# Kernel tuning notes

Hardware: AMD Instinct MI355X
Metric: run time of the kernel (lower is better)

Reference implementation:

```python
import jax, jax.numpy as jnp
import numpy as np

N, D, P, NS = 2048, 64, 32, 512  # nnodes, stop_embedding_size, preference_dim, n_active_stops
LEAKY_SLOPE = 0.01
COS_EPS = 1e-8


def setup_inputs() -> dict:
    key = jax.random.key(0)
    ks = jax.random.split(key, 10)
    dist = jax.random.uniform(ks[0], (N, N), dtype=jnp.float32)
    stops = jax.random.randint(ks[1], (NS,), 0, N)
    emb_w = jax.random.normal(ks[2], (N, D), dtype=jnp.float32) * 0.05      # nn.Embedding weight
    lin_l_w = jax.random.normal(ks[3], (P, D), dtype=jnp.float32) * 0.05    # SAGEConv lin_l (aggregated)
    lin_l_b = jnp.zeros((P,), dtype=jnp.float32)
    lin_r_w = jax.random.normal(ks[4], (P, D), dtype=jnp.float32) * 0.05    # SAGEConv lin_r (root)
    edge_w = jax.random.normal(ks[5], (2 * P,), dtype=jnp.float32) * 0.05   # edge_summarizer weight
    edge_b = jnp.zeros((), dtype=jnp.float32)
    in_len = 2 * N + 3 + P
    comb_w = jax.random.normal(ks[6], (N, in_len), dtype=jnp.float32) * 0.02  # combiner weight
    comb_b = jnp.zeros((N,), dtype=jnp.float32)
    return {
        "dist": dist, "emb_w": emb_w,
        "lin_l_w": lin_l_w, "lin_l_b": lin_l_b, "lin_r_w": lin_r_w,
        "edge_w": edge_w, "edge_b": edge_b,
        "comb_w": comb_w, "comb_b": comb_b,
        "stops": stops, "weekday": 3, "vehicles": 5,
    }


def reference(dist, emb_w, lin_l_w, lin_l_b, lin_r_w, edge_w, edge_b,
              comb_w, comb_b, stops, weekday, vehicles):
    dt = emb_w.dtype
    # --- cosine-similarity graph build ---
    norm = jnp.maximum(jnp.linalg.norm(emb_w, axis=1, keepdims=True), COS_EPS)
    xn = emb_w / norm
    sim = xn @ xn.T                                   # [N, N]
    sim = sim * (1.0 - jnp.eye(N, dtype=dt))          # fill_diagonal_(0)
    keep = jnp.zeros((N,), dtype=bool).at[stops].set(True)
    adj = ((sim > 0.5) & keep[:, None] & keep[None, :]).astype(dt)  # [N, N]
    # --- SAGEConv (mean aggregation): lin_l(mean_j x_j) + lin_r(x_i) ---
    deg = jnp.maximum(adj.sum(axis=1, keepdims=True), 1.0)
    agg = (adj @ emb_w) / deg                         # [N, D]
    pref = agg @ lin_l_w.T + lin_l_b + emb_w @ lin_r_w.T   # [N, P]
    # --- all-pairs edge summaries: Linear([pref_i, pref_j]) + LeakyReLU ---
    # equivalent to concat-then-linear, without materializing [N^2, 2P]
    a = pref @ edge_w[:P]                             # [N]
    b = pref @ edge_w[P:]                             # [N]
    es = a[:, None] + b[None, :] + edge_b             # [N, N]
    es = jnp.where(es >= 0, es, LEAKY_SLOPE * es)
    # --- combiner + log-softmax ---
    weekday_feat = jnp.full((N, 1), weekday, dtype=dt)
    vehicle_feat = jnp.full((N, 1), vehicles, dtype=dt)
    stop_feat = keep.astype(dt)[:, None]
    combined = jnp.concatenate([pref, es, dist, weekday_feat, vehicle_feat, stop_feat], axis=1)
    out = combined @ comb_w.T + comb_b                # [N, N]
    return jax.nn.log_softmax(out, axis=1)
```

## Files before the change

### kernel.cpp

```cpp
#include <hip/hip_runtime.h>

typedef unsigned short u16;
typedef __attribute__((ext_vector_type(8))) short bf16x8;
typedef __attribute__((ext_vector_type(4))) float f32x4;

__device__ __forceinline__ u16 f2bf(float f) {
    return (u16)((__float_as_uint(f) + 0x8000u) >> 16);
}

#define N_NODES 2048
#define D_EMB 64
#define P_DIM 32
#define NS_STOPS 512
#define IN_LEN 4131
#define NKT 65
#define NKTA 33

#define SWZ(row, c) ((((row) * 8) + ((c) ^ ((row) & 7))) * 8)

__device__ __forceinline__ void gload16(const u16* g, u16* l) {
    __builtin_amdgcn_global_load_lds((const __attribute__((address_space(1))) void*)g,
                                     (__attribute__((address_space(3))) void*)l, 16, 0, 0);
}

__global__ __launch_bounds__(256) void k_aggpref(const float* __restrict__ emb, const int* __restrict__ stops,
                                                 const float* __restrict__ lin_l_w, const float* __restrict__ lin_l_b,
                                                 const float* __restrict__ lin_r_w, const float* __restrict__ edge_w,
                                                 float* __restrict__ pref, float* __restrict__ av, float* __restrict__ bv) {
    __shared__ float se[NS_STOPS][68];
    __shared__ int bm[64];
    __shared__ int kl[NS_STOPS];
    __shared__ float nrm[NS_STOPS];
    __shared__ float xiS[8][D_EMB];
    __shared__ float aggS[8][D_EMB];
    __shared__ float niS[8];
    __shared__ int degS[8];
    __shared__ int kiS[8];
    __shared__ int cnt;
    int t = threadIdx.x;
    int i0 = blockIdx.x * 8;
    if (t < 64) bm[t] = 0;
    if (t == 0) cnt = 0;
    if (t < 8) degS[t] = 0;
    ((float*)aggS)[t] = 0.f;
    ((float*)aggS)[t + 256] = 0.f;
    __syncthreads();
    {
        int s0 = stops[t], s1 = stops[t + 256];
        atomicOr(&bm[s0 >> 5], 1 << (s0 & 31));
        atomicOr(&bm[s1 >> 5], 1 << (s1 & 31));
    }
    __syncthreads();
    {
        int w = bm[t >> 2];
        int base = (t >> 2) * 32 + (t & 3) * 8;
        #pragma unroll
        for (int e = 0; e < 8; ++e)
            if ((w >> ((t & 3) * 8 + e)) & 1) { int p = atomicAdd(&cnt, 1); kl[p] = base + e; }
    }
    if (t < 8) { int i = i0 + t; kiS[t] = (bm[i >> 5] >> (i & 31)) & 1; }
    {
        int n = t >> 5, d = (t & 31) * 2;
        xiS[n][d]     = emb[(i0 + n) * D_EMB + d];
        xiS[n][d + 1] = emb[(i0 + n) * D_EMB + d + 1];
    }
    __syncthreads();
    int nk = cnt;
    for (int u = t >> 3; u < nk; u += 32) {
        int l8 = (t & 7) * 8;
        f32x4 a = *(const f32x4*)&emb[kl[u] * D_EMB + l8];
        f32x4 b = *(const f32x4*)&emb[kl[u] * D_EMB + l8 + 4];
        *(f32x4*)&se[u][l8] = a;
        *(f32x4*)&se[u][l8 + 4] = b;
    }
    if (t < 8) {
        float s = 0.f;
        #pragma unroll
        for (int d = 0; d < D_EMB; ++d) s += xiS[t][d] * xiS[t][d];
        niS[t] = fmaxf(sqrtf(s), 1e-8f);
    }
    __syncthreads();
    for (int u = t; u < nk; u += 256) {
        float s = 0.f;
        #pragma unroll
        for (int d = 0; d < 16; ++d) {
            f32x4 v = *(const f32x4*)&se[u][d * 4];
            s += v[0] * v[0] + v[1] * v[1] + v[2] * v[2] + v[3] * v[3];
        }
        nrm[u] = fmaxf(sqrtf(s), 1e-8f);
    }
    __syncthreads();
    for (int u = t; u < nk; u += 256) {
        int j = kl[u];
        float nj = nrm[u];
        f32x4 er[16];
        #pragma unroll
        for (int d = 0; d < 16; ++d) er[d] = *(const f32x4*)&se[u][d * 4];
        #pragma unroll
        for (int n = 0; n < 8; ++n) {
            if (!kiS[n] || j == i0 + n) continue;
            f32x4 dv = {0.f, 0.f, 0.f, 0.f};
            #pragma unroll
            for (int d = 0; d < 16; ++d) dv += (*(const f32x4*)&xiS[n][d * 4]) * er[d];
            float dot = dv[0] + dv[1] + dv[2] + dv[3];
            if (dot > 0.5f * niS[n] * nj) {
                atomicAdd(&degS[n], 1);
                #pragma unroll
                for (int d = 0; d < 16; ++d) {
                    atomicAdd(&aggS[n][d * 4 + 0], er[d][0]);
                    atomicAdd(&aggS[n][d * 4 + 1], er[d][1]);
                    atomicAdd(&aggS[n][d * 4 + 2], er[d][2]);
                    atomicAdd(&aggS[n][d * 4 + 3], er[d][3]);
                }
            }
        }
    }
    __syncthreads();
    {
        int n = t >> 5, p = t & 31;
        int i = i0 + n;
        float inv = kiS[n] ? (1.f / fmaxf((float)degS[n], 1.0f)) : 0.f;
        float s = lin_l_b[p];
        const float* wl = &lin_l_w[p * D_EMB];
        const float* wr = &lin_r_w[p * D_EMB];
        #pragma unroll
        for (int d = 0; d < D_EMB; ++d) s += aggS[n][d] * inv * wl[d] + xiS[n][d] * wr[d];
        pref[i * P_DIM + p] = s;
        float a = s * edge_w[p];
        float b = s * edge_w[P_DIM + p];
        #pragma unroll
        for (int off = 16; off; off >>= 1) { a += __shfl_xor(a, off, 32); b += __shfl_xor(b, off, 32); }
        if (p == 0) { av[i] = a; bv[i] = b; }
    }
}

__global__ __launch_bounds__(256) void k_pack(const float* __restrict__ comb_w, const float* __restrict__ comb_b,
                                              const int* __restrict__ wk_p, const int* __restrict__ vh_p,
                                              const float* __restrict__ dist, const float* __restrict__ pref,
                                              u16* __restrict__ Bp, u16* __restrict__ Ap,
                                              float* __restrict__ cvec, float* __restrict__ w3) {
    int kt = blockIdx.x;
    int ty = blockIdx.y;
    int t = threadIdx.x;
    if (ty < 16) {
        int nt = ty;
        u16* tb = Bp + ((size_t)nt * NKT + kt) * 8192;
        #pragma unroll
        for (int it = 0; it < 4; ++it) {
            int q = t + it * 256;
            int r = q >> 3, c = q & 7;
            int j = nt * 128 + r;
            int k0 = kt * 64 + c * 8;
            const float* cw = comb_w + (size_t)j * IN_LEN;
            bf16x8 v;
            if (k0 < 4096) {
                f32x4 f0, f1;
                __builtin_memcpy(&f0, cw + 32 + k0, 16);
                __builtin_memcpy(&f1, cw + 36 + k0, 16);
                #pragma unroll
                for (int e = 0; e < 4; ++e) { v[e] = (short)f2bf(f0[e]); v[4 + e] = (short)f2bf(f1[e]); }
            } else if (k0 < 4128) {
                f32x4 f0, f1;
                __builtin_memcpy(&f0, cw + (k0 - 4096), 16);
                __builtin_memcpy(&f1, cw + (k0 - 4092), 16);
                #pragma unroll
                for (int e = 0; e < 4; ++e) { v[e] = (short)f2bf(f0[e]); v[4 + e] = (short)f2bf(f1[e]); }
            } else {
                #pragma unroll
                for (int e = 0; e < 8; ++e) v[e] = 0;
            }
            *(bf16x8*)&tb[r * 64 + ((c ^ (r & 7)) * 8)] = v;
        }
        if (kt == 64 && t < 128) {
            int j = nt * 128 + t;
            const float* cw = comb_w + (size_t)j * IN_LEN;
            float wk = (float)wk_p[0], vh = (float)vh_p[0];
            cvec[j] = wk * cw[4128] + vh * cw[4129] + comb_b[j];
            w3[j] = cw[4130];
        }
    } else {
        if (kt < 32) return;
        int rt = ty - 16;
        u16* ta = Ap + ((size_t)rt * NKTA + (kt - 32)) * 4096;
        #pragma unroll
        for (int it = 0; it < 2; ++it) {
            int q = t + it * 256;
            int r = q >> 3, c = q & 7;
            int row = rt * 64 + r;
            int k0 = kt * 64 + c * 8;
            bf16x8 v;
            if (k0 < 4096) {
                const f32x4* dp = (const f32x4*)(dist + (size_t)row * 2048 + (k0 - 2048));
                f32x4 f0 = dp[0], f1 = dp[1];
                #pragma unroll
                for (int e = 0; e < 4; ++e) { v[e] = (short)f2bf(f0[e]); v[4 + e] = (short)f2bf(f1[e]); }
            } else if (k0 < 4128) {
                const f32x4* pp = (const f32x4*)(pref + (size_t)row * P_DIM + (k0 - 4096));
                f32x4 f0 = pp[0], f1 = pp[1];
                #pragma unroll
                for (int e = 0; e < 4; ++e) { v[e] = (short)f2bf(f0[e]); v[4 + e] = (short)f2bf(f1[e]); }
            } else {
                #pragma unroll
                for (int e = 0; e < 8; ++e) v[e] = 0;
            }
            *(bf16x8*)&ta[r * 64 + ((c ^ (r & 7)) * 8)] = v;
        }
    }
}

__global__ __launch_bounds__(256, 4) void k_gemm_d(const u16* __restrict__ Ap, const u16* __restrict__ Bp,
                                                   const float* __restrict__ av, const float* __restrict__ bv,
                                                   const float* __restrict__ edge_b,
                                                   float* __restrict__ Cout) {
    __shared__ __attribute__((aligned(16))) short As[2][4096];
    __shared__ __attribute__((aligned(16))) short Bs[2][4096];
    int t = threadIdx.x;
    int b = blockIdx.x;
    int c = b & 7, u = b >> 3;
    int mt = (c & 1) * 16 + (u & 15);
    int nt = (c >> 1) * 8 + (u >> 4);
    int tileM = mt * 64, tileN = nt * 64;
    int lane = t & 63;
    int wid = t >> 6;
    int waveM = wid & 1, waveN = wid >> 1;
    int l16 = lane & 15, quad = lane >> 4;
    int r_ = t >> 2;
    float avr = av[tileM + r_] + edge_b[0];

    f32x4 acc[2][2];
    #pragma unroll
    for (int a_ = 0; a_ < 2; ++a_)
        #pragma unroll
        for (int b_ = 0; b_ < 2; ++b_) acc[a_][b_] = (f32x4){0.f, 0.f, 0.f, 0.f};

    const u16* gB = Bp + ((size_t)(nt >> 1) * NKT) * 8192 + (nt & 1) * 4096 + t * 8;
    const u16* gA = Ap + ((size_t)mt * NKTA) * 4096 + t * 8;

#define ISSUE(ktv, bb) do { \
        const u16* b0 = gB + (size_t)(ktv) * 8192; \
        u16* bd = (u16*)Bs[bb] + t * 8; \
        gload16(b0, bd); \
        gload16(b0 + 2048, bd + 2048); \
        if ((ktv) < 32) { \
            int k0 = (ktv) * 64; \
            _Pragma("unroll") \
            for (int cc = 0; cc < 2; ++cc) { \
                int ch = (t & 3) * 2 + cc; \
                f32x4 f0 = *(const f32x4*)&bv[k0 + ch * 8]; \
                f32x4 f1 = *(const f32x4*)&bv[k0 + ch * 8 + 4]; \
                bf16x8 v; \
                _Pragma("unroll") \
                for (int e = 0; e < 4; ++e) { \
                    float s0 = avr + f0[e]; s0 = (s0 >= 0.f) ? s0 : 0.01f * s0; \
                    float s1 = avr + f1[e]; s1 = (s1 >= 0.f) ? s1 : 0.01f * s1; \
                    v[e] = (short)f2bf(s0); v[4 + e] = (short)f2bf(s1); \
                } \
                *(bf16x8*)&As[bb][SWZ(r_, ch)] = v; \
            } \
        } else { \
            const u16* a0 = gA + (size_t)((ktv) - 32) * 4096; \
            u16* ad = (u16*)As[bb] + t * 8; \
            gload16(a0, ad); \
            gload16(a0 + 2048, ad + 2048); \
        } \
    } while (0)

    ISSUE(0, 0);

    int cur = 0;
    for (int kt = 0; kt < NKT; ++kt) {
        __syncthreads();
        if (kt + 1 < NKT) ISSUE(kt + 1, cur ^ 1);
        const short* Asc = As[cur];
        const short* Bsc = Bs[cur];
        #pragma unroll
        for (int kk = 0; kk < 64; kk += 32) {
            int cbase = kk >> 3;
            bf16x8 af[2], bfr[2];
            #pragma unroll
            for (int mi = 0; mi < 2; ++mi) {
                int row = waveM * 32 + mi * 16 + l16;
                af[mi] = *(const bf16x8*)&Asc[SWZ(row, cbase + quad)];
            }
            #pragma unroll
            for (int ni = 0; ni < 2; ++ni) {
                int row = waveN * 32 + ni * 16 + l16;
                bfr[ni] = *(const bf16x8*)&Bsc[SWZ(row, cbase + quad)];
            }
            #pragma unroll
            for (int mi = 0; mi < 2; ++mi)
                #pragma unroll
                for (int ni = 0; ni < 2; ++ni)
                    acc[mi][ni] = __builtin_amdgcn_mfma_f32_16x16x32_bf16(af[mi], bfr[ni], acc[mi][ni], 0, 0, 0);
        }
        cur ^= 1;
    }
#undef ISSUE
    #pragma unroll
    for (int mi = 0; mi < 2; ++mi)
        #pragma unroll
        for (int ni = 0; ni < 2; ++ni) {
            int row = tileM + waveM * 32 + mi * 16 + quad * 4;
            int col = tileN + waveN * 32 + ni * 16 + l16;
            float* cp = Cout + (size_t)row * N_NODES + col;
            #pragma unroll
            for (int rr = 0; rr < 4; ++rr) cp[(size_t)rr * N_NODES] = acc[mi][ni][rr];
        }
}

__global__ __launch_bounds__(256) void k_epi(const float* __restrict__ cvec, const float* __restrict__ w3,
                                             const int* __restrict__ stops, float* __restrict__ out) {
    int i = blockIdx.x, t = threadIdx.x;
    __shared__ int bm[64];
    __shared__ float redmax[4], redsum[4];
    if (t < 64) bm[t] = 0;
    __syncthreads();
    {
        int s0 = stops[t], s1 = stops[t + 256];
        atomicOr(&bm[s0 >> 5], 1 << (s0 & 31));
        atomicOr(&bm[s1 >> 5], 1 << (s1 & 31));
    }
    __syncthreads();
    float ki = (float)((bm[i >> 5] >> (i & 31)) & 1);
    f32x4* orow = (f32x4*)(out + (size_t)i * N_NODES);
    const f32x4* cv = (const f32x4*)cvec;
    const f32x4* wv = (const f32x4*)w3;
    f32x4 v0 = orow[t] + cv[t] + ki * wv[t];
    f32x4 v1 = orow[t + 256] + cv[t + 256] + ki * wv[t + 256];
    float vmax = fmaxf(fmaxf(fmaxf(v0[0], v0[1]), fmaxf(v0[2], v0[3])),
                       fmaxf(fmaxf(v1[0], v1[1]), fmaxf(v1[2], v1[3])));
    #pragma unroll
    for (int off = 32; off; off >>= 1) vmax = fmaxf(vmax, __shfl_xor(vmax, off, 64));
    if ((t & 63) == 0) redmax[t >> 6] = vmax;
    __syncthreads();
    vmax = fmaxf(fmaxf(redmax[0], redmax[1]), fmaxf(redmax[2], redmax[3]));
    float se = 0.f;
    #pragma unroll
    for (int e = 0; e < 4; ++e) se += expf(v0[e] - vmax) + expf(v1[e] - vmax);
    #pragma unroll
    for (int off = 32; off; off >>= 1) se += __shfl_xor(se, off, 64);
    if ((t & 63) == 0) redsum[t >> 6] = se;
    __syncthreads();
    se = redsum[0] + redsum[1] + redsum[2] + redsum[3];
    float lz = vmax + logf(se);
    orow[t] = v0 - lz;
    orow[t + 256] = v1 - lz;
}

extern "C" void kernel_launch(void* const* d_in, const int* in_sizes, int n_in,
                              void* d_out, int out_size, void* d_ws, size_t ws_size,
                              hipStream_t stream) {
    const float* dist    = (const float*)d_in[0];
    const float* emb     = (const float*)d_in[1];
    const float* lin_l_w = (const float*)d_in[2];
    const float* lin_l_b = (const float*)d_in[3];
    const float* lin_r_w = (const float*)d_in[4];
    const float* edge_w  = (const float*)d_in[5];
    const float* edge_b  = (const float*)d_in[6];
    const float* comb_w  = (const float*)d_in[7];
    const float* comb_b  = (const float*)d_in[8];
    const int* stops     = (const int*)d_in[9];
    const int* wk        = (const int*)d_in[10];
    const int* vh        = (const int*)d_in[11];

    char* ws = (char*)d_ws;
    float* pref  = (float*)(ws + 0);
    float* av    = (float*)(ws + 262144);
    float* bv    = (float*)(ws + 270336);
    float* cvec  = (float*)(ws + 278528);
    float* w3    = (float*)(ws + 286720);
    u16*   Ap    = (u16*)(ws + 294912);
    u16*   Bp    = (u16*)(ws + 8945664);
    float* out   = (float*)d_out;

    hipLaunchKernelGGL(k_aggpref, dim3(256),    dim3(256), 0, stream, emb, stops,
                       lin_l_w, lin_l_b, lin_r_w, edge_w, pref, av, bv);
    hipLaunchKernelGGL(k_pack,    dim3(65, 48), dim3(256), 0, stream, comb_w, comb_b, wk, vh,
                       dist, pref, Bp, Ap, cvec, w3);
    hipLaunchKernelGGL(k_gemm_d,  dim3(1024),   dim3(256), 0, stream, Ap, Bp, av, bv, edge_b, out);
    hipLaunchKernelGGL(k_epi,     dim3(2048),   dim3(256), 0, stream, cvec, w3, stops, out);
}
```

Before: 206.1 us.

## Pre-pack edge-summary A tiles in pack kernel and fuse bias into GEMM epilogue

The LeakyReLU edge-summary tiles were built in registers inside the GEMM main loop. They are now materialised as bf16 swizzled tiles in the pack kernel, so every k-step of the GEMM issues uniform async global-to-LDS loads. The bias vector and the stop-flag column term move from the softmax kernel into the GEMM store, and the per-row keep flag is written by the aggregation kernel. The trade is a packed A buffer about twice as large, with the extra global writes and reads that come with it, in exchange for a simpler GEMM inner loop and a lighter epilogue kernel.

```diff
diff --git a/kernel.cpp b/kernel.cpp
--- a/kernel.cpp
+++ b/kernel.cpp
@@ -14,7 +14,6 @@
 #define NS_STOPS 512
 #define IN_LEN 4131
 #define NKT 65
-#define NKTA 33
 
 #define SWZ(row, c) ((((row) * 8) + ((c) ^ ((row) & 7))) * 8)
 
@@ -26,7 +25,8 @@
 __global__ __launch_bounds__(256) void k_aggpref(const float* __restrict__ emb, const int* __restrict__ stops,
                                                  const float* __restrict__ lin_l_w, const float* __restrict__ lin_l_b,
                                                  const float* __restrict__ lin_r_w, const float* __restrict__ edge_w,
-                                                 float* __restrict__ pref, float* __restrict__ av, float* __restrict__ bv) {
+                                                 float* __restrict__ pref, float* __restrict__ av, float* __restrict__ bv,
+                                                 float* __restrict__ keepf) {
     __shared__ float se[NS_STOPS][68];
     __shared__ int bm[64];
     __shared__ int kl[NS_STOPS];
@@ -130,13 +130,15 @@
         float b = s * edge_w[P_DIM + p];
         #pragma unroll
         for (int off = 16; off; off >>= 1) { a += __shfl_xor(a, off, 32); b += __shfl_xor(b, off, 32); }
-        if (p == 0) { av[i] = a; bv[i] = b; }
+        if (p == 0) { av[i] = a; bv[i] = b; keepf[i] = (float)kiS[n]; }
     }
 }
 
 __global__ __launch_bounds__(256) void k_pack(const float* __restrict__ comb_w, const float* __restrict__ comb_b,
                                               const int* __restrict__ wk_p, const int* __restrict__ vh_p,
                                               const float* __restrict__ dist, const float* __restrict__ pref,
+                                              const float* __restrict__ av, const float* __restrict__ bv,
+                                              const float* __restrict__ edge_b,
                                               u16* __restrict__ Bp, u16* __restrict__ Ap,
                                               float* __restrict__ cvec, float* __restrict__ w3) {
     int kt = blockIdx.x;
@@ -179,9 +181,9 @@
             w3[j] = cw[4130];
         }
     } else {
-        if (kt < 32) return;
         int rt = ty - 16;
-        u16* ta = Ap + ((size_t)rt * NKTA + (kt - 32)) * 4096;
+        u16* ta = Ap + ((size_t)rt * NKT + kt) * 4096;
+        float eb = edge_b[0];
         #pragma unroll
         for (int it = 0; it < 2; ++it) {
             int q = t + it * 256;
@@ -189,7 +191,17 @@
             int row = rt * 64 + r;
             int k0 = kt * 64 + c * 8;
             bf16x8 v;
-            if (k0 < 4096) {
+            if (k0 < 2048) {
+                float ab = av[row] + eb;
+                f32x4 f0 = *(const f32x4*)(bv + k0);
+                f32x4 f1 = *(const f32x4*)(bv + k0 + 4);
+                #pragma unroll
+                for (int e = 0; e < 4; ++e) {
+                    float s0 = ab + f0[e]; s0 = (s0 >= 0.f) ? s0 : 0.01f * s0;
+                    float s1 = ab + f1[e]; s1 = (s1 >= 0.f) ? s1 : 0.01f * s1;
+                    v[e] = (short)f2bf(s0); v[4 + e] = (short)f2bf(s1);
+                }
+            } else if (k0 < 4096) {
                 const f32x4* dp = (const f32x4*)(dist + (size_t)row * 2048 + (k0 - 2048));
                 f32x4 f0 = dp[0], f1 = dp[1];
                 #pragma unroll
@@ -209,8 +221,8 @@
 }
 
 __global__ __launch_bounds__(256, 4) void k_gemm_d(const u16* __restrict__ Ap, const u16* __restrict__ Bp,
-                                                   const float* __restrict__ av, const float* __restrict__ bv,
-                                                   const float* __restrict__ edge_b,
+                                                   const float* __restrict__ cvec, const float* __restrict__ w3,
+                                                   const float* __restrict__ keepf,
                                                    float* __restrict__ Cout) {
     __shared__ __attribute__((aligned(16))) short As[2][4096];
     __shared__ __attribute__((aligned(16))) short Bs[2][4096];
@@ -224,8 +236,6 @@
     int wid = t >> 6;
     int waveM = wid & 1, waveN = wid >> 1;
     int l16 = lane & 15, quad = lane >> 4;
-    int r_ = t >> 2;
-    float avr = av[tileM + r_] + edge_b[0];
 
     f32x4 acc[2][2];
     #pragma unroll
@@ -233,36 +243,18 @@
         #pragma unroll
         for (int b_ = 0; b_ < 2; ++b_) acc[a_][b_] = (f32x4){0.f, 0.f, 0.f, 0.f};
 
+    const u16* gA = Ap + ((size_t)mt * NKT) * 4096 + t * 8;
     const u16* gB = Bp + ((size_t)(nt >> 1) * NKT) * 8192 + (nt & 1) * 4096 + t * 8;
-    const u16* gA = Ap + ((size_t)mt * NKTA) * 4096 + t * 8;
 
 #define ISSUE(ktv, bb) do { \
+        const u16* a0 = gA + (size_t)(ktv) * 4096; \
         const u16* b0 = gB + (size_t)(ktv) * 8192; \
+        u16* ad = (u16*)As[bb] + t * 8; \
         u16* bd = (u16*)Bs[bb] + t * 8; \
+        gload16(a0, ad); \
+        gload16(a0 + 2048, ad + 2048); \
         gload16(b0, bd); \
         gload16(b0 + 2048, bd + 2048); \
-        if ((ktv) < 32) { \
-            int k0 = (ktv) * 64; \
-            _Pragma("unroll") \
-            for (int cc = 0; cc < 2; ++cc) { \
-                int ch = (t & 3) * 2 + cc; \
-                f32x4 f0 = *(const f32x4*)&bv[k0 + ch * 8]; \
-                f32x4 f1 = *(const f32x4*)&bv[k0 + ch * 8 + 4]; \
-                bf16x8 v; \
-                _Pragma("unroll") \
-                for (int e = 0; e < 4; ++e) { \
-                    float s0 = avr + f0[e]; s0 = (s0 >= 0.f) ? s0 : 0.01f * s0; \
-                    float s1 = avr + f1[e]; s1 = (s1 >= 0.f) ? s1 : 0.01f * s1; \
-                    v[e] = (short)f2bf(s0); v[4 + e] = (short)f2bf(s1); \
-                } \
-                *(bf16x8*)&As[bb][SWZ(r_, ch)] = v; \
-            } \
-        } else { \
-            const u16* a0 = gA + (size_t)((ktv) - 32) * 4096; \
-            u16* ad = (u16*)As[bb] + t * 8; \
-            gload16(a0, ad); \
-            gload16(a0 + 2048, ad + 2048); \
-        } \
     } while (0)
 
     ISSUE(0, 0);
@@ -300,33 +292,22 @@
     for (int mi = 0; mi < 2; ++mi)
         #pragma unroll
         for (int ni = 0; ni < 2; ++ni) {
-            int row = tileM + waveM * 32 + mi * 16 + quad * 4;
+            int row0 = tileM + waveM * 32 + mi * 16 + quad * 4;
             int col = tileN + waveN * 32 + ni * 16 + l16;
-            float* cp = Cout + (size_t)row * N_NODES + col;
-            #pragma unroll
-            for (int rr = 0; rr < 4; ++rr) cp[(size_t)rr * N_NODES] = acc[mi][ni][rr];
-        }
-}
-
-__global__ __launch_bounds__(256) void k_epi(const float* __restrict__ cvec, const float* __restrict__ w3,
-                                             const int* __restrict__ stops, float* __restrict__ out) {
+            float cv = cvec[col], wv = w3[col];
+            float* cp = Cout + (size_t)row0 * N_NODES + col;
+            #pragma unroll
+            for (int rr = 0; rr < 4; ++rr)
+                cp[(size_t)rr * N_NODES] = acc[mi][ni][rr] + cv + keepf[row0 + rr] * wv;
+        }
+}
+
+__global__ __launch_bounds__(256) void k_epi(float* __restrict__ out) {
     int i = blockIdx.x, t = threadIdx.x;
-    __shared__ int bm[64];
     __shared__ float redmax[4], redsum[4];
-    if (t < 64) bm[t] = 0;
-    __syncthreads();
-    {
-        int s0 = stops[t], s1 = stops[t + 256];
-        atomicOr(&bm[s0 >> 5], 1 << (s0 & 31));
-        atomicOr(&bm[s1 >> 5], 1 << (s1 & 31));
-    }
-    __syncthreads();
-    float ki = (float)((bm[i >> 5] >> (i & 31)) & 1);
     f32x4* orow = (f32x4*)(out + (size_t)i * N_NODES);
-    const f32x4* cv = (const f32x4*)cvec;
-    const f32x4* wv = (const f32x4*)w3;
-    f32x4 v0 = orow[t] + cv[t] + ki * wv[t];
-    f32x4 v1 = orow[t + 256] + cv[t + 256] + ki * wv[t + 256];
+    f32x4 v0 = orow[t];
+    f32x4 v1 = orow[t + 256];
     float vmax = fmaxf(fmaxf(fmaxf(v0[0], v0[1]), fmaxf(v0[2], v0[3])),
                        fmaxf(fmaxf(v1[0], v1[1]), fmaxf(v1[2], v1[3])));
     #pragma unroll
@@ -369,14 +350,15 @@
     float* bv    = (float*)(ws + 270336);
     float* cvec  = (float*)(ws + 278528);
     float* w3    = (float*)(ws + 286720);
-    u16*   Ap    = (u16*)(ws + 294912);
-    u16*   Bp    = (u16*)(ws + 8945664);
+    float* keepf = (float*)(ws + 294912);
+    u16*   Ap    = (u16*)(ws + 303104);
+    u16*   Bp    = (u16*)(ws + 17342464);
     float* out   = (float*)d_out;
 
     hipLaunchKernelGGL(k_aggpref, dim3(256),    dim3(256), 0, stream, emb, stops,
-                       lin_l_w, lin_l_b, lin_r_w, edge_w, pref, av, bv);
+                       lin_l_w, lin_l_b, lin_r_w, edge_w, pref, av, bv, keepf);
     hipLaunchKernelGGL(k_pack,    dim3(65, 48), dim3(256), 0, stream, comb_w, comb_b, wk, vh,
-                       dist, pref, Bp, Ap, cvec, w3);
-    hipLaunchKernelGGL(k_gemm_d,  dim3(1024),   dim3(256), 0, stream, Ap, Bp, av, bv, edge_b, out);
-    hipLaunchKernelGGL(k_epi,     dim3(2048),   dim3(256), 0, stream, cvec, w3, stops, out);
-}
+                       dist, pref, av, bv, edge_b, Bp, Ap, cvec, w3);
+    hipLaunchKernelGGL(k_gemm_d,  dim3(1024),   dim3(256), 0, stream, Ap, Bp, cvec, w3, keepf, out);
+    hipLaunchKernelGGL(k_epi,     dim3(2048),   dim3(256), 0, stream, out);
+}
```

New measurement: 188.8 us. -8.4%, faster.
